# Kernel optimization log

Hardware: AMD Instinct MI355X
Metric: run time of the kernel (lower is better)

## Reference

```python
import jax, jax.numpy as jnp
import numpy as np

B = 4
MAX_N = 2048
D = 512
H = 8
HD = D // H
SRC_LENS = [2048, 1536, 1800, 1200]   # sum = 6584
REF_LENS = [1900, 2048, 1400, 1600]   # sum = 6948
NEG_INF = -1e9


def setup_inputs() -> dict:
    key = jax.random.key(0)
    ks = jax.random.split(key, 8)
    n_src, n_ref = sum(SRC_LENS), sum(REF_LENS)
    s = 0.02
    return {
        "feats_src": jax.random.normal(ks[0], (n_src, D), dtype=jnp.float32),
        "batch_src": jnp.asarray(np.repeat(np.arange(B), SRC_LENS), dtype=jnp.int32),
        "feats_ref": jax.random.normal(ks[1], (n_ref, D), dtype=jnp.float32),
        "batch_ref": jnp.asarray(np.repeat(np.arange(B), REF_LENS), dtype=jnp.int32),
        "w_in": jax.random.normal(ks[2], (3 * D, D), dtype=jnp.float32) * s,
        "b_in": jnp.zeros((3 * D,), dtype=jnp.float32),
        "w_out": jax.random.normal(ks[3], (D, D), dtype=jnp.float32) * s,
        "b_out": jnp.zeros((D,), dtype=jnp.float32),
        "gw1": jax.random.normal(ks[4], (D, D), dtype=jnp.float32) * s,
        "gb1": jnp.zeros((D,), dtype=jnp.float32),
        "gw2": jax.random.normal(ks[5], (1, D), dtype=jnp.float32) * s,
        "gb2": jnp.zeros((1,), dtype=jnp.float32),
    }


def _to_dense(feats, batch_idx):
    # sparse [N, D] (sorted batch indices) -> dense [B, MAX_N, D] + key_padding_mask
    n = feats.shape[0]
    counts = jax.ops.segment_sum(jnp.ones((n,), jnp.int32), batch_idx, num_segments=B)
    starts = jnp.concatenate([jnp.zeros((1,), jnp.int32), jnp.cumsum(counts)[:-1].astype(jnp.int32)])
    pos = jnp.arange(n, dtype=jnp.int32) - starts[batch_idx]  # position within batch
    dense = jnp.zeros((B, MAX_N, feats.shape[1]), feats.dtype).at[batch_idx, pos].set(feats)
    mask = jnp.arange(MAX_N)[None, :] >= counts[:, None]  # True = padding (key_padding_mask)
    return dense, mask, pos


def reference(feats_src, batch_src, feats_ref, batch_ref,
              w_in, b_in, w_out, b_out, gw1, gb1, gw2, gb2):
    d_src, mask_src, pos_src = _to_dense(feats_src, batch_src)
    d_ref, mask_ref, _ = _to_dense(feats_ref, batch_ref)

    # nn.MultiheadAttention (batch_first, eval mode): packed in_proj, scaled dot-product
    q = (d_src @ w_in[:D].T + b_in[:D]).reshape(B, MAX_N, H, HD)
    k = (d_ref @ w_in[D:2 * D].T + b_in[D:2 * D]).reshape(B, MAX_N, H, HD)
    v = (d_ref @ w_in[2 * D:].T + b_in[2 * D:]).reshape(B, MAX_N, H, HD)
    scores = jnp.einsum('bqhd,bkhd->bhqk', q * (HD ** -0.5), k)
    scores = jnp.where(mask_ref[:, None, None, :], NEG_INF, scores)
    attn = jax.nn.softmax(scores, axis=-1)
    ctx = jnp.einsum('bhqk,bkhd->bqhd', attn, v).reshape(B, MAX_N, D)
    d_aligned = ctx @ w_out.T + b_out

    # gate MLP: Linear -> ReLU -> Linear -> Sigmoid
    gate = jax.nn.sigmoid(jax.nn.relu(d_aligned @ gw1.T + gb1) @ gw2.T + gb2)  # [B, MAX_N, 1]
    d_out = d_src + gate * d_aligned

    # dense -> ragged: gather each token back to its flat slot
    out_flat = d_out[batch_src, pos_src]  # [N_src, D]
    return out_flat, gate
```

## Files before the change

kernel.cpp:

```cpp
#include <hip/hip_runtime.h>
#include <hip/hip_bf16.h>


typedef __bf16 bf16x8_t __attribute__((ext_vector_type(8)));
typedef __bf16 bf16x4_t __attribute__((ext_vector_type(4)));
typedef float f32x4_t __attribute__((ext_vector_type(4)));
typedef float f32x2_t __attribute__((ext_vector_type(2)));

#define CQ_SCALE 0.18033688011112042f

__device__ inline bf16x8_t zero8() {
  bf16x8_t z;
#pragma unroll
  for (int t = 0; t < 8; ++t) z[t] = (__bf16)0.0f;
  return z;
}

__device__ __forceinline__ int sniff_f32(const void* w) {
  unsigned short u = ((const unsigned short*)w)[threadIdx.x & 63];
  return __ballot((u & 0x7F80) >= 0x3F80) != 0ULL;
}

__global__ void sentinel_k(float* out) {
  if (threadIdx.x == 0 && blockIdx.x == 0) out[0] = 1000.0f;
}

__global__ void cv_all(const void* w_in, const void* b_in, const void* w_out,
                       const void* b_out, const void* gw1, const void* gb1,
                       const void* gw2, const void* gb2,
                       __hip_bfloat16* __restrict__ ws) {
  int f = sniff_f32(w_in);
  const size_t F_W_IN = 16, F_B_IN = 786448, F_W_OUT = 787984, F_B_OUT = 1050128,
               F_GW1 = 1050640, F_GB1 = 1312784, F_GW2 = 1313296, F_GB2 = 1313808;
  const int total = 1313793;
  for (int g = blockIdx.x * 256 + threadIdx.x; g < total; g += gridDim.x * 256) {
    const void* src;
    size_t dst;
    int i;
    if (g < 786432) { src = w_in; dst = F_W_IN; i = g; }
    else if (g < 787968) { src = b_in; dst = F_B_IN; i = g - 786432; }
    else if (g < 1050112) { src = w_out; dst = F_W_OUT; i = g - 787968; }
    else if (g < 1050624) { src = b_out; dst = F_B_OUT; i = g - 1050112; }
    else if (g < 1312768) { src = gw1; dst = F_GW1; i = g - 1050624; }
    else if (g < 1313280) { src = gb1; dst = F_GB1; i = g - 1312768; }
    else if (g < 1313792) { src = gw2; dst = F_GW2; i = g - 1313280; }
    else { src = gb2; dst = F_GB2; i = g - 1313792; }
    ws[dst + i] = f ? __float2bfloat16(((const float*)src)[i])
                    : ((const __hip_bfloat16*)src)[i];
  }
}

__device__ __forceinline__ void gemm_core(
    const void* __restrict__ A_, long aoff, const __hip_bfloat16* __restrict__ Bt,
    const __hip_bfloat16* __restrict__ bias, __hip_bfloat16* __restrict__ C,
    int M, int K, int lda, int ldc, float cscale, int relu, int f, int bm, int bn,
    long chs, __bf16 (&As)[128][72], __bf16 (&Bs)[128][72]) {
  int tid = threadIdx.x, lane = tid & 63, wave = tid >> 6;
  int wm = wave >> 1, wn = wave & 1;
  int l15 = lane & 15, quad = lane >> 4;

  f32x4_t acc[4][4];
#pragma unroll
  for (int i = 0; i < 4; ++i)
#pragma unroll
    for (int j = 0; j < 4; ++j)
#pragma unroll
      for (int r = 0; r < 4; ++r) acc[i][j][r] = 0.f;

  bf16x8_t ra[4], rb[4];
  f32x4_t raf[4][2];

  auto gload = [&](int k0) {
#pragma unroll
    for (int s = 0; s < 4; ++s) {
      int id = s * 256 + tid;
      int row = id >> 3, col = (id & 7) * 8;
      int arow = bm + row;
      if (f) {
        if (arow < M) {
          const float* p = (const float*)A_ + aoff + (size_t)arow * lda + k0 + col;
          raf[s][0] = *reinterpret_cast<const f32x4_t*>(p);
          raf[s][1] = *reinterpret_cast<const f32x4_t*>(p + 4);
        } else {
#pragma unroll
          for (int e = 0; e < 4; ++e) { raf[s][0][e] = 0.f; raf[s][1][e] = 0.f; }
        }
      } else {
        ra[s] = (arow < M)
                    ? *reinterpret_cast<const bf16x8_t*>((const __hip_bfloat16*)A_ + aoff +
                                                         (size_t)arow * lda + k0 + col)
                    : zero8();
      }
      rb[s] = *reinterpret_cast<const bf16x8_t*>(Bt + (size_t)(bn + row) * 512 + k0 + col);
    }
  };
  auto stage = [&]() {
#pragma unroll
    for (int s = 0; s < 4; ++s) {
      int id = s * 256 + tid;
      int row = id >> 3, col = (id & 7) * 8;
      if (f) {
        bf16x8_t t;
#pragma unroll
        for (int e = 0; e < 4; ++e) {
          t[e] = (__bf16)raf[s][0][e];
          t[4 + e] = (__bf16)raf[s][1][e];
        }
        *reinterpret_cast<bf16x8_t*>(&As[row][col]) = t;
      } else {
        *reinterpret_cast<bf16x8_t*>(&As[row][col]) = ra[s];
      }
      *reinterpret_cast<bf16x8_t*>(&Bs[row][col]) = rb[s];
    }
  };

  int nk = K >> 6;
  gload(0);
  for (int it = 0; it < nk; ++it) {
    stage();
    __syncthreads();
    if (it + 1 < nk) gload((it + 1) * 64);
#pragma unroll
    for (int ks = 0; ks < 2; ++ks) {
      bf16x8_t af[4], bfv[4];
#pragma unroll
      for (int i = 0; i < 4; ++i)
        af[i] = *reinterpret_cast<const bf16x8_t*>(
            &As[wm * 64 + i * 16 + l15][ks * 32 + quad * 8]);
#pragma unroll
      for (int j = 0; j < 4; ++j)
        bfv[j] = *reinterpret_cast<const bf16x8_t*>(
            &Bs[wn * 64 + j * 16 + l15][ks * 32 + quad * 8]);
#pragma unroll
      for (int i = 0; i < 4; ++i)
#pragma unroll
        for (int j = 0; j < 4; ++j)
          acc[i][j] = __builtin_amdgcn_mfma_f32_16x16x32_bf16(af[i], bfv[j], acc[i][j], 0, 0, 0);
    }
    __syncthreads();
  }

#pragma unroll
  for (int i = 0; i < 4; ++i)
#pragma unroll
    for (int j = 0; j < 4; ++j) {
      int col = bn + wn * 64 + j * 16 + l15;
      float bv = __bfloat162float(bias[col]);
#pragma unroll
      for (int r = 0; r < 4; ++r) {
        int row = bm + wm * 64 + i * 16 + quad * 4 + r;
        if (row < M) {
          float v = (acc[i][j][r] + bv) * cscale;
          if (relu) v = fmaxf(v, 0.f);
          size_t idx = chs ? ((size_t)(col >> 6) * chs + (size_t)row * 64 + (col & 63))
                           : ((size_t)row * ldc + col);
          C[idx] = __float2bfloat16(v);
        }
      }
    }
}

__global__ __launch_bounds__(256) void proj2(
    const void* __restrict__ fs, const void* __restrict__ fr,
    const __hip_bfloat16* __restrict__ ws, __hip_bfloat16* __restrict__ Q,
    __hip_bfloat16* __restrict__ KV, const void* snf) {
  __shared__ __bf16 As[128][72];
  __shared__ __bf16 Bs[128][72];
  const size_t F_W_IN = 16, F_B_IN = 786448;
  const long CHS = (long)6948 * 64;
  int f = sniff_f32(snf);
  int bid = blockIdx.x;
  if (bid < 208) {
    int bx = bid >> 2, by = bid & 3;
    gemm_core(fs, 0, ws + F_W_IN, ws + F_B_IN, Q, 6584, 512, 512, 512, CQ_SCALE, 0, f,
              bx * 128, by * 128, 0, As, Bs);
  } else {
    int k = bid - 208;
    int bx = k >> 3, by = k & 7;
    gemm_core(fr, 0, ws + F_W_IN + 262144, ws + F_B_IN + 512, KV, 6948, 512, 512, 1024,
              1.0f, 0, f, bx * 128, by * 128, CHS, As, Bs);
  }
}

template <bool AF32>
__global__ __launch_bounds__(256) void gemm128(
    const void* __restrict__ A_, long aoff, const __hip_bfloat16* __restrict__ Bt,
    const __hip_bfloat16* __restrict__ bias, __hip_bfloat16* __restrict__ C,
    int M, int K, int lda, int ldc, float cscale, int relu, long chs,
    const void* snf) {
  __shared__ __bf16 As[128][72];
  __shared__ __bf16 Bs[128][72];
  int f = 0;
  if constexpr (AF32) f = sniff_f32(snf);
  gemm_core(A_, aoff, Bt, bias, C, M, K, lda, ldc, cscale, relu, f,
            blockIdx.x * 128, blockIdx.y * 128, chs, As, Bs);
}

template <int NS>
__global__ __launch_bounds__(256) void gemm128_pv(
    const __hip_bfloat16* __restrict__ P, const float* __restrict__ L,
    const __hip_bfloat16* __restrict__ Bt, const __hip_bfloat16* __restrict__ bias,
    __hip_bfloat16* __restrict__ C, int M) {
  const size_t PSZ = 3375104;
  __shared__ __bf16 As[128][72];
  __shared__ __bf16 Bs[128][72];
  int tid = threadIdx.x, lane = tid & 63, wave = tid >> 6;
  int wm = wave >> 1, wn = wave & 1;
  int l15 = lane & 15, quad = lane >> 4;
  int bm = blockIdx.x * 128, bn = blockIdx.y * 128;

  f32x4_t acc[4][4];
#pragma unroll
  for (int i = 0; i < 4; ++i)
#pragma unroll
    for (int j = 0; j < 4; ++j)
#pragma unroll
      for (int r = 0; r < 4; ++r) acc[i][j][r] = 0.f;

  bf16x8_t rp[NS][4], rb[4];
  float rl[4][NS];

  auto gload = [&](int k0) {
    int h = k0 >> 6;
#pragma unroll
    for (int s = 0; s < 4; ++s) {
      int id = s * 256 + tid;
      int row = id >> 3, col = (id & 7) * 8;
      int arow = bm + row;
      if (arow < M) {
        size_t off = (size_t)arow * 512 + k0 + col;
#pragma unroll
        for (int i = 0; i < NS; ++i)
          rp[i][s] = *reinterpret_cast<const bf16x8_t*>(P + i * PSZ + off);
        const float* lp = &L[((size_t)arow * 8 + h) * NS];
#pragma unroll
        for (int i = 0; i < NS; ++i) rl[s][i] = lp[i];
      } else {
#pragma unroll
        for (int i = 0; i < NS; ++i) rp[i][s] = zero8();
        rl[s][0] = 1.f;
#pragma unroll
        for (int i = 1; i < NS; ++i) rl[s][i] = 0.f;
      }
      rb[s] = *reinterpret_cast<const bf16x8_t*>(Bt + (size_t)(bn + row) * 512 + k0 + col);
    }
  };
  auto stage = [&]() {
#pragma unroll
    for (int s = 0; s < 4; ++s) {
      int id = s * 256 + tid;
      int row = id >> 3, col = (id & 7) * 8;
      float sum = 0.f;
#pragma unroll
      for (int i = 0; i < NS; ++i) sum += rl[s][i];
      float sc = 1.0f / sum;
      bf16x8_t t;
#pragma unroll
      for (int e = 0; e < 8; ++e) {
        float v = 0.f;
#pragma unroll
        for (int i = 0; i < NS; ++i) v += rl[s][i] * (float)rp[i][s][e];
        t[e] = (__bf16)(v * sc);
      }
      *reinterpret_cast<bf16x8_t*>(&As[row][col]) = t;
      *reinterpret_cast<bf16x8_t*>(&Bs[row][col]) = rb[s];
    }
  };

  gload(0);
  for (int it = 0; it < 8; ++it) {
    stage();
    __syncthreads();
    if (it + 1 < 8) gload((it + 1) * 64);
#pragma unroll
    for (int ks = 0; ks < 2; ++ks) {
      bf16x8_t af[4], bfv[4];
#pragma unroll
      for (int i = 0; i < 4; ++i)
        af[i] = *reinterpret_cast<const bf16x8_t*>(
            &As[wm * 64 + i * 16 + l15][ks * 32 + quad * 8]);
#pragma unroll
      for (int j = 0; j < 4; ++j)
        bfv[j] = *reinterpret_cast<const bf16x8_t*>(
            &Bs[wn * 64 + j * 16 + l15][ks * 32 + quad * 8]);
#pragma unroll
      for (int i = 0; i < 4; ++i)
#pragma unroll
        for (int j = 0; j < 4; ++j)
          acc[i][j] = __builtin_amdgcn_mfma_f32_16x16x32_bf16(af[i], bfv[j], acc[i][j], 0, 0, 0);
    }
    __syncthreads();
  }

#pragma unroll
  for (int i = 0; i < 4; ++i)
#pragma unroll
    for (int j = 0; j < 4; ++j) {
      int col = bn + wn * 64 + j * 16 + l15;
      float bv = __bfloat162float(bias[col]);
#pragma unroll
      for (int r = 0; r < 4; ++r) {
        int row = bm + wm * 64 + i * 16 + quad * 4 + r;
        if (row < M)
          C[(size_t)row * 512 + col] = __float2bfloat16(acc[i][j][r] + bv);
      }
    }
}

__device__ __forceinline__ void flash_core(
    const __hip_bfloat16* __restrict__ Qb, const __hip_bfloat16* __restrict__ Kb,
    const __hip_bfloat16* __restrict__ Vb, __hip_bfloat16* __restrict__ OUTb,
    float* __restrict__ LPb, int lns, int nsrc, int nref, int qt, int kt0,
    int ktNfull, int do_tail, __bf16 (&KsL)[2][64][68], __bf16 (&VtL)[2][64][72],
    __bf16 (&PL)[4][32][68]) {
  int h = blockIdx.y;
  int tid = threadIdx.x, lane = tid & 63, wave = tid >> 6;
  int l15 = lane & 15, quad = lane >> 4;
  int Mb = nsrc + 1;
  int qbase = qt * 128 + wave * 32;

  bf16x8_t qfr[2][2];
#pragma unroll
  for (int g = 0; g < 2; ++g) {
    int qrow = qbase + g * 16 + l15;
#pragma unroll
    for (int ks = 0; ks < 2; ++ks)
      qfr[g][ks] = (qrow < nsrc)
                       ? *reinterpret_cast<const bf16x8_t*>(
                             Qb + (size_t)qrow * 512 + h * 64 + ks * 32 + quad * 8)
                       : zero8();
  }

  f32x4_t O[2][4];
#pragma unroll
  for (int g = 0; g < 2; ++g)
#pragma unroll
    for (int j = 0; j < 4; ++j)
#pragma unroll
      for (int r = 0; r < 4; ++r) O[g][j][r] = 0.f;

  f32x4_t Lacc[2];
#pragma unroll
  for (int g = 0; g < 2; ++g)
#pragma unroll
    for (int r = 0; r < 4; ++r) Lacc[g][r] = 0.f;
  bf16x8_t ones;
#pragma unroll
  for (int t = 0; t < 8; ++t) ones[t] = (__bf16)1.0f;

  auto load64pair = [&](const __bf16* p) {
    bf16x4_t lo = *reinterpret_cast<const bf16x4_t*>(p);
    bf16x4_t hi = *reinterpret_cast<const bf16x4_t*>(p + 4);
    bf16x8_t v;
#pragma unroll
    for (int e = 0; e < 4; ++e) {
      v[e] = lo[e];
      v[4 + e] = hi[e];
    }
    return v;
  };

  bf16x8_t krA[2], v0, v1;
  auto gloadK = [&](int k0) {
    const __hip_bfloat16* base = Kb + (size_t)k0 * 64 + tid * 16;
    krA[0] = *reinterpret_cast<const bf16x8_t*>(base);
    krA[1] = *reinterpret_cast<const bf16x8_t*>(base + 8);
  };
  auto stageK = [&](int buf) {
#pragma unroll
    for (int p = 0; p < 2; ++p) {
      int lin = tid * 16 + p * 8;
      int row = lin >> 6, col = lin & 63;
      *reinterpret_cast<bf16x4_t*>(&KsL[buf][row][col]) =
          *reinterpret_cast<const bf16x4_t*>(&krA[p]);
      bf16x4_t hi;
#pragma unroll
      for (int e = 0; e < 4; ++e) hi[e] = krA[p][4 + e];
      *reinterpret_cast<bf16x4_t*>(&KsL[buf][row][col + 4]) = hi;
    }
  };
  auto loadV = [&](int k0) {
    const __hip_bfloat16* vp = Vb + (size_t)(k0 + lane) * 64 + wave * 16;
    v0 = *reinterpret_cast<const bf16x8_t*>(vp);
    v1 = *reinterpret_cast<const bf16x8_t*>(vp + 8);
  };

  int nit = ktNfull - kt0;
  if (nit > 0) {
    gloadK(kt0 * 64);
    loadV(kt0 * 64);
  }

  int buf = 0;
  for (int it = 0; it < nit; ++it) {
    int k0 = (kt0 + it) * 64;
    stageK(buf);
    {
      __bf16(*Vt)[72] = VtL[buf];
#pragma unroll
      for (int e = 0; e < 8; ++e) {
        Vt[wave * 16 + e][lane] = v0[e];
        Vt[wave * 16 + 8 + e][lane] = v1[e];
      }
    }
    __syncthreads();
    if (it + 1 < nit) {
      gloadK(k0 + 64);
      loadV(k0 + 64);
    }

    bf16x8_t kf[8];
#pragma unroll
    for (int j = 0; j < 4; ++j)
#pragma unroll
      for (int ks = 0; ks < 2; ++ks)
        kf[j * 2 + ks] = load64pair(&KsL[buf][j * 16 + l15][ks * 32 + quad * 8]);
#pragma unroll
    for (int g = 0; g < 2; ++g) {
      f32x4_t St[4];
#pragma unroll
      for (int j = 0; j < 4; ++j)
#pragma unroll
        for (int r = 0; r < 4; ++r) St[j][r] = 0.f;
#pragma unroll
      for (int j = 0; j < 4; ++j)
#pragma unroll
        for (int ks = 0; ks < 2; ++ks)
          St[j] = __builtin_amdgcn_mfma_f32_16x16x32_bf16(kf[j * 2 + ks], qfr[g][ks],
                                                          St[j], 0, 0, 0);
#pragma unroll
      for (int j = 0; j < 4; ++j) {
        bf16x4_t pk;
#pragma unroll
        for (int r = 0; r < 4; ++r) pk[r] = (__bf16)exp2f(St[j][r]);
        *reinterpret_cast<bf16x4_t*>(&PL[wave][g * 16 + l15][j * 16 + quad * 4]) = pk;
      }
    }

    bf16x8_t pa[2][2];
#pragma unroll
    for (int g = 0; g < 2; ++g)
#pragma unroll
      for (int ks = 0; ks < 2; ++ks)
        pa[g][ks] = load64pair(&PL[wave][g * 16 + l15][ks * 32 + quad * 8]);
#pragma unroll
    for (int g = 0; g < 2; ++g)
#pragma unroll
      for (int ks = 0; ks < 2; ++ks)
        Lacc[g] = __builtin_amdgcn_mfma_f32_16x16x32_bf16(pa[g][ks], ones, Lacc[g], 0, 0, 0);
#pragma unroll
    for (int j = 0; j < 4; ++j)
#pragma unroll
      for (int ks = 0; ks < 2; ++ks) {
        bf16x8_t vbf = *reinterpret_cast<const bf16x8_t*>(
            &VtL[buf][j * 16 + l15][ks * 32 + quad * 8]);
#pragma unroll
        for (int g = 0; g < 2; ++g)
          O[g][j] = __builtin_amdgcn_mfma_f32_16x16x32_bf16(pa[g][ks], vbf, O[g][j], 0, 0, 0);
      }
    __syncthreads();
    buf ^= 1;
  }

  if (do_tail) {
    int k0 = ktNfull * 64;
    __bf16(*Vt)[72] = VtL[buf];
    {
      int kr = k0 + lane;
      const __hip_bfloat16* vp = Vb + (size_t)kr * 64 + wave * 16;
      bf16x8_t t0 = (kr < nref) ? *reinterpret_cast<const bf16x8_t*>(vp) : zero8();
      bf16x8_t t1 = (kr < nref) ? *reinterpret_cast<const bf16x8_t*>(vp + 8) : zero8();
#pragma unroll
      for (int e = 0; e < 8; ++e) {
        Vt[wave * 16 + e][lane] = t0[e];
        Vt[wave * 16 + 8 + e][lane] = t1[e];
      }
    }
    bf16x8_t kf[8];
#pragma unroll
    for (int j = 0; j < 4; ++j) {
      int kcol = k0 + j * 16 + l15;
      const __hip_bfloat16* kp = Kb + (size_t)kcol * 64 + quad * 8;
      kf[j * 2] = (kcol < nref) ? *reinterpret_cast<const bf16x8_t*>(kp) : zero8();
      kf[j * 2 + 1] = (kcol < nref) ? *reinterpret_cast<const bf16x8_t*>(kp + 32) : zero8();
    }
#pragma unroll
    for (int g = 0; g < 2; ++g) {
      f32x4_t St[4];
#pragma unroll
      for (int j = 0; j < 4; ++j)
#pragma unroll
        for (int r = 0; r < 4; ++r) St[j][r] = 0.f;
#pragma unroll
      for (int j = 0; j < 4; ++j)
#pragma unroll
        for (int ks = 0; ks < 2; ++ks)
          St[j] = __builtin_amdgcn_mfma_f32_16x16x32_bf16(kf[j * 2 + ks], qfr[g][ks],
                                                          St[j], 0, 0, 0);
#pragma unroll
      for (int j = 0; j < 4; ++j) {
        bf16x4_t pk;
#pragma unroll
        for (int r = 0; r < 4; ++r) {
          int kl = k0 + j * 16 + quad * 4 + r;
          pk[r] = (__bf16)((kl < nref) ? exp2f(St[j][r]) : 0.f);
        }
        *reinterpret_cast<bf16x4_t*>(&PL[wave][g * 16 + l15][j * 16 + quad * 4]) = pk;
      }
    }
    __syncthreads();
    bf16x8_t pa[2][2];
#pragma unroll
    for (int g = 0; g < 2; ++g)
#pragma unroll
      for (int ks = 0; ks < 2; ++ks)
        pa[g][ks] = load64pair(&PL[wave][g * 16 + l15][ks * 32 + quad * 8]);
#pragma unroll
    for (int g = 0; g < 2; ++g)
#pragma unroll
      for (int ks = 0; ks < 2; ++ks)
        Lacc[g] = __builtin_amdgcn_mfma_f32_16x16x32_bf16(pa[g][ks], ones, Lacc[g], 0, 0, 0);
#pragma unroll
    for (int j = 0; j < 4; ++j)
#pragma unroll
      for (int ks = 0; ks < 2; ++ks) {
        bf16x8_t vbf =
            *reinterpret_cast<const bf16x8_t*>(&Vt[j * 16 + l15][ks * 32 + quad * 8]);
#pragma unroll
        for (int g = 0; g < 2; ++g)
          O[g][j] = __builtin_amdgcn_mfma_f32_16x16x32_bf16(pa[g][ks], vbf, O[g][j], 0, 0, 0);
      }
  }

  if (LPb && l15 == 0) {
#pragma unroll
    for (int g = 0; g < 2; ++g)
#pragma unroll
      for (int r = 0; r < 4; ++r) {
        int row = qbase + g * 16 + quad * 4 + r;
        if (row < Mb) LPb[((size_t)row * 8 + h) * lns] = Lacc[g][r];
      }
  }

#pragma unroll
  for (int g = 0; g < 2; ++g)
#pragma unroll
    for (int r = 0; r < 4; ++r) {
      int row = qbase + g * 16 + quad * 4 + r;
      if (row < Mb) {
        float inv = 1.0f / Lacc[g][r];
#pragma unroll
        for (int j = 0; j < 4; ++j)
          OUTb[(size_t)row * 512 + h * 64 + j * 16 + l15] =
              __float2bfloat16(O[g][j][r] * inv);
      }
    }
}

__global__ __launch_bounds__(256, 3) void flash_all(
    const __hip_bfloat16* __restrict__ Q, const __hip_bfloat16* __restrict__ KV,
    __hip_bfloat16* __restrict__ P, float* __restrict__ L, int nsplit) {
  const int TILE_START[4] = {0, 17, 30, 45};
  const int SRC_START[4] = {0, 2048, 3584, 5384};
  const int REF_START[4] = {0, 1900, 3948, 5348};
  const int SRC_LEN[4] = {2048, 1536, 1800, 1200};
  const int REF_LEN[4] = {1900, 2048, 1400, 1600};
  const int CS[4] = {0, 2049, 3586, 5387};
  const size_t PSZ = 3375104;
  const size_t CHS = (size_t)6948 * 64;
  __shared__ __bf16 KsL[2][64][68];
  __shared__ __bf16 VtL[2][64][72];
  __shared__ __bf16 PL[4][32][68];
  int bid = blockIdx.x;
  int b = (bid >= TILE_START[3]) ? 3 : (bid >= TILE_START[2]) ? 2 : (bid >= TILE_START[1]) ? 1 : 0;
  int qt = bid - TILE_START[b];
  int nref = REF_LEN[b];
  int full = nref >> 6, nkt = (nref + 63) >> 6, rem = nref & 63;
  int split = blockIdx.z;
  int kt0 = (nkt * split) / nsplit;
  int ktN, tail;
  if (split == nsplit - 1) { ktN = full; tail = rem > 0; }
  else { ktN = (nkt * (split + 1)) / nsplit; tail = 0; }
  int h = blockIdx.y;
  const __hip_bfloat16* Kb = KV + (size_t)h * CHS + (size_t)REF_START[b] * 64;
  const __hip_bfloat16* Vb = KV + (size_t)(8 + h) * CHS + (size_t)REF_START[b] * 64;
  __hip_bfloat16* OUT = P + (size_t)split * PSZ;
  float* LP = (nsplit == 1) ? nullptr : (L + split + (size_t)CS[b] * 8 * nsplit);
  flash_core(Q + (size_t)SRC_START[b] * 512, Kb, Vb, OUT + (size_t)CS[b] * 512, LP,
             nsplit, SRC_LEN[b], nref, qt, kt0, ktN, tail, KsL, VtL, PL);
}

__global__ __launch_bounds__(256, 3) void flash_one(const __hip_bfloat16* __restrict__ Qb,
                                                    const __hip_bfloat16* __restrict__ KVb,
                                                    __hip_bfloat16* __restrict__ OUTb,
                                                    int nsrc, int nref, long chs) {
  __shared__ __bf16 KsL[2][64][68];
  __shared__ __bf16 VtL[2][64][72];
  __shared__ __bf16 PL[4][32][68];
  int h = blockIdx.y;
  const __hip_bfloat16* Kb = KVb + (size_t)h * chs;
  const __hip_bfloat16* Vb = KVb + (size_t)(8 + h) * chs;
  flash_core(Qb, Kb, Vb, OUTb, nullptr, 1, nsrc, nref, blockIdx.x, 0, nref >> 6,
             (nref & 63) > 0, KsL, VtL, PL);
}

__global__ __launch_bounds__(256) void finalize_all(
    const void* __restrict__ src, const __hip_bfloat16* __restrict__ aligned,
    const __hip_bfloat16* __restrict__ hidden, const __hip_bfloat16* __restrict__ gw2,
    const __hip_bfloat16* __restrict__ gb2, void* __restrict__ out, const void* snf) {
  int f = sniff_f32(snf);
  int lane = threadIdx.x & 63;
  int r = blockIdx.x * 4 + (threadIdx.x >> 6);
  int b = (r >= 5387) ? 3 : (r >= 3586) ? 2 : (r >= 2049) ? 1 : 0;
  const int CS[4] = {0, 2049, 3586, 5387};
  const int NSRC[4] = {2048, 1536, 1800, 1200};
  int pos = r - CS[b];

  float zacc = 0.f;
  const __hip_bfloat16* hrow = hidden + (size_t)r * 512;
#pragma unroll
  for (int t = 0; t < 8; ++t) {
    int c = lane + (t << 6);
    zacc += __bfloat162float(hrow[c]) * __bfloat162float(gw2[c]);
  }
  for (int o = 32; o; o >>= 1) zacc += __shfl_xor(zacc, o);
  zacc += __bfloat162float(gb2[0]);
  float g = 1.f / (1.f + __expf(-zacc));

  const size_t GOFF = (size_t)6584 * 512;
  if (pos < NSRC[b]) {
    size_t ib = (size_t)(r - b) * 512;
    const __hip_bfloat16* arow = aligned + (size_t)r * 512;
#pragma unroll
    for (int t = 0; t < 8; ++t) {
      int c = lane + (t << 6);
      float sv = f ? ((const float*)src)[ib + c]
                   : __bfloat162float(((const __hip_bfloat16*)src)[ib + c]);
      float val = sv + g * __bfloat162float(arow[c]);
      if (f) ((float*)out)[ib + c] = val;
      else ((__hip_bfloat16*)out)[ib + c] = __float2bfloat16(val);
    }
    if (lane == 0) {
      size_t go = GOFF + b * 2048 + pos;
      if (f) ((float*)out)[go] = g;
      else ((__hip_bfloat16*)out)[go] = __float2bfloat16(g);
    }
  } else {
    for (int p = NSRC[b] + lane; p < 2048; p += 64) {
      size_t go = GOFF + b * 2048 + p;
      if (f) ((float*)out)[go] = g;
      else ((__hip_bfloat16*)out)[go] = __float2bfloat16(g);
    }
  }
}

__global__ __launch_bounds__(256) void finalize_b(
    const void* __restrict__ src, const __hip_bfloat16* __restrict__ alnb,
    const __hip_bfloat16* __restrict__ hidb, const __hip_bfloat16* __restrict__ gw2,
    const __hip_bfloat16* __restrict__ gb2, void* __restrict__ out,
    int b, int nsrc, int src_start, const void* snf) {
  int f = sniff_f32(snf);
  int lane = threadIdx.x & 63;
  int r = blockIdx.x * 4 + (threadIdx.x >> 6);
  if (r > nsrc) return;

  float zacc = 0.f;
  const __hip_bfloat16* hrow = hidb + (size_t)r * 512;
#pragma unroll
  for (int t = 0; t < 8; ++t) {
    int c = lane + (t << 6);
    zacc += __bfloat162float(hrow[c]) * __bfloat162float(gw2[c]);
  }
  for (int o = 32; o; o >>= 1) zacc += __shfl_xor(zacc, o);
  zacc += __bfloat162float(gb2[0]);
  float g = 1.f / (1.f + __expf(-zacc));

  const size_t GOFF = (size_t)6584 * 512;
  if (r < nsrc) {
    size_t ib = (size_t)(src_start + r) * 512;
    const __hip_bfloat16* arow = alnb + (size_t)r * 512;
#pragma unroll
    for (int t = 0; t < 8; ++t) {
      int c = lane + (t << 6);
      float sv = f ? ((const float*)src)[ib + c]
                   : __bfloat162float(((const __hip_bfloat16*)src)[ib + c]);
      float val = sv + g * __bfloat162float(arow[c]);
      if (f) ((float*)out)[ib + c] = val;
      else ((__hip_bfloat16*)out)[ib + c] = __float2bfloat16(val);
    }
    if (lane == 0) {
      size_t go = GOFF + b * 2048 + r;
      if (f) ((float*)out)[go] = g;
      else ((__hip_bfloat16*)out)[go] = __float2bfloat16(g);
    }
  } else {
    for (int p = nsrc + lane; p < 2048; p += 64) {
      size_t go = GOFF + b * 2048 + p;
      if (f) ((float*)out)[go] = g;
      else ((__hip_bfloat16*)out)[go] = __float2bfloat16(g);
    }
  }
}

extern "C" void kernel_launch(void* const* d_in, const int* in_sizes, int n_in,
                              void* d_out, int out_size, void* d_ws, size_t ws_size,
                              hipStream_t stream) {
  (void)in_sizes; (void)n_in; (void)out_size;
  const void* feats_src = d_in[0];
  const void* feats_ref = d_in[2];
  const void* w_in = d_in[4];
  const void* b_in = d_in[5];
  const void* w_out = d_in[6];
  const void* b_out = d_in[7];
  const void* gw1 = d_in[8];
  const void* gb1 = d_in[9];
  const void* gw2 = d_in[10];
  const void* gb2 = d_in[11];

  const size_t F_W_IN = 16, F_B_IN = 786448, F_W_OUT = 787984, F_B_OUT = 1050128,
               F_GW1 = 1050640, F_GB1 = 1312784, F_GW2 = 1313296, F_GB2 = 1313808,
               A0 = 1313824;
  const size_t PSZ = 3375104;
  const size_t R3E = A0 + PSZ + 7114752;
  const size_t NEED_A2 = 2 * (R3E + 2 * PSZ + 210816);
  const size_t NEED_A = 2 * (R3E + PSZ);
  const size_t NEED_B = 2 * (A0 + 4259840);

  if (ws_size < NEED_B) {
    sentinel_k<<<1, 64, 0, stream>>>((float*)d_out);
    return;
  }

  __hip_bfloat16* ws = (__hip_bfloat16*)d_ws;
  cv_all<<<dim3(1024), dim3(256), 0, stream>>>(w_in, b_in, w_out, b_out, gw1, gb1, gw2,
                                               gb2, ws);

  const int SRC_LEN[4] = {2048, 1536, 1800, 1200};
  const int REF_LEN[4] = {1900, 2048, 1400, 1600};
  const int SRC_START[4] = {0, 2048, 3584, 5384};
  const int REF_START[4] = {0, 1900, 3948, 5348};
  dim3 blk(256);

  if (ws_size >= NEED_A) {
    __hip_bfloat16* R1 = ws + A0;
    __hip_bfloat16* R2 = R1 + PSZ;
    __hip_bfloat16* R3 = R2 + 7114752;
    proj2<<<dim3(648), blk, 0, stream>>>(feats_src, feats_ref, ws, R1, R2, w_in);
    int NS = (ws_size >= NEED_A2) ? 2 : 1;
    if (NS == 2) {
      float* L = (float*)(ws + R3E + 2 * PSZ);
      flash_all<<<dim3(55, 8, 2), blk, 0, stream>>>(R1, R2, R3, L, 2);
      gemm128_pv<2><<<dim3(52, 4), blk, 0, stream>>>(R3, L, ws + F_W_OUT,
                                                     ws + F_B_OUT, R1, 6588);
    } else {
      flash_all<<<dim3(55, 8, 1), blk, 0, stream>>>(R1, R2, R3, nullptr, 1);
      gemm128<false><<<dim3(52, 4), blk, 0, stream>>>(R3, 0, ws + F_W_OUT, ws + F_B_OUT,
                                                      R1, 6588, 512, 512, 512, 1.0f, 0,
                                                      0, nullptr);
    }
    gemm128<false><<<dim3(52, 4), blk, 0, stream>>>(R1, 0, ws + F_GW1, ws + F_GB1, R3,
                                                    6588, 512, 512, 512, 1.0f, 1, 0,
                                                    nullptr);
    finalize_all<<<dim3(1647), blk, 0, stream>>>(feats_src, R1, R3, ws + F_GW2,
                                                 ws + F_GB2, d_out, w_in);
  } else {
    __hip_bfloat16* W2 = ws + A0;
    __hip_bfloat16* W1 = W2 + 2097152;
    __hip_bfloat16* W3 = W1 + 1081344;
    const long CHS_B = (long)2048 * 64;
    for (int b = 0; b < 4; ++b) {
      int nsrc = SRC_LEN[b], nref = REF_LEN[b];
      gemm128<true><<<dim3((nsrc + 127) / 128, 4), blk, 0, stream>>>(
          feats_src, (long)SRC_START[b] * 512, ws + F_W_IN, ws + F_B_IN, W1, nsrc, 512,
          512, 512, CQ_SCALE, 0, 0, w_in);
      gemm128<true><<<dim3((nref + 127) / 128, 8), blk, 0, stream>>>(
          feats_ref, (long)REF_START[b] * 512, ws + F_W_IN + 262144, ws + F_B_IN + 512,
          W2, nref, 512, 512, 1024, 1.0f, 0, CHS_B, w_in);
      flash_one<<<dim3((nsrc + 128) / 128, 8), blk, 0, stream>>>(W1, W2, W3, nsrc, nref,
                                                                 CHS_B);
      gemm128<false><<<dim3((nsrc + 128) / 128, 4), blk, 0, stream>>>(
          W3, 0, ws + F_W_OUT, ws + F_B_OUT, W1, nsrc + 1, 512, 512, 512, 1.0f, 0, 0,
          nullptr);
      gemm128<false><<<dim3((nsrc + 128) / 128, 4), blk, 0, stream>>>(
          W1, 0, ws + F_GW1, ws + F_GB1, W3, nsrc + 1, 512, 512, 512, 1.0f, 1, 0,
          nullptr);
      finalize_b<<<dim3((nsrc + 4) / 4), blk, 0, stream>>>(
          feats_src, W1, W3, ws + F_GW2, ws + F_GB2, d_out, b, nsrc, SRC_START[b], w_in);
    }
  }
}
```

Baseline: 236.6 us.

## Shrink GEMM N-tile to 64 and split flash launch by batch pairs

Changes every GEMM tile from 128x128 to 128x64, with each of the four waves owning 32 rows. Grids double and the kernels get launch_bounds min-blocks of 4, so more blocks fit on the GPU and occupancy rises on these small-M GEMMs. The flash attention launch is split into two launches, one per pair of batches, with the tile-to-batch lookup rewritten to match. The cost is less B-operand reuse per block, more redundant A loads, and one extra kernel launch.

```diff
diff --git a/kernel.cpp b/kernel.cpp
--- a/kernel.cpp
+++ b/kernel.cpp
@@ -54,20 +54,19 @@
     const void* __restrict__ A_, long aoff, const __hip_bfloat16* __restrict__ Bt,
     const __hip_bfloat16* __restrict__ bias, __hip_bfloat16* __restrict__ C,
     int M, int K, int lda, int ldc, float cscale, int relu, int f, int bm, int bn,
-    long chs, __bf16 (&As)[128][72], __bf16 (&Bs)[128][72]) {
+    long chs, __bf16 (&As)[128][72], __bf16 (&Bs)[64][72]) {
   int tid = threadIdx.x, lane = tid & 63, wave = tid >> 6;
-  int wm = wave >> 1, wn = wave & 1;
   int l15 = lane & 15, quad = lane >> 4;
 
-  f32x4_t acc[4][4];
-#pragma unroll
-  for (int i = 0; i < 4; ++i)
+  f32x4_t acc[2][4];
+#pragma unroll
+  for (int i = 0; i < 2; ++i)
 #pragma unroll
     for (int j = 0; j < 4; ++j)
 #pragma unroll
       for (int r = 0; r < 4; ++r) acc[i][j][r] = 0.f;
 
-  bf16x8_t ra[4], rb[4];
+  bf16x8_t ra[4], rb[2];
   f32x4_t raf[4][2];
 
   auto gload = [&](int k0) {
@@ -91,6 +90,11 @@
                                                          (size_t)arow * lda + k0 + col)
                     : zero8();
       }
+    }
+#pragma unroll
+    for (int s = 0; s < 2; ++s) {
+      int id = s * 256 + tid;
+      int row = id >> 3, col = (id & 7) * 8;
       rb[s] = *reinterpret_cast<const bf16x8_t*>(Bt + (size_t)(bn + row) * 512 + k0 + col);
     }
   };
@@ -110,6 +114,11 @@
       } else {
         *reinterpret_cast<bf16x8_t*>(&As[row][col]) = ra[s];
       }
+    }
+#pragma unroll
+    for (int s = 0; s < 2; ++s) {
+      int id = s * 256 + tid;
+      int row = id >> 3, col = (id & 7) * 8;
       *reinterpret_cast<bf16x8_t*>(&Bs[row][col]) = rb[s];
     }
   };
@@ -122,17 +131,17 @@
     if (it + 1 < nk) gload((it + 1) * 64);
 #pragma unroll
     for (int ks = 0; ks < 2; ++ks) {
-      bf16x8_t af[4], bfv[4];
-#pragma unroll
-      for (int i = 0; i < 4; ++i)
+      bf16x8_t af[2], bfv[4];
+#pragma unroll
+      for (int i = 0; i < 2; ++i)
         af[i] = *reinterpret_cast<const bf16x8_t*>(
-            &As[wm * 64 + i * 16 + l15][ks * 32 + quad * 8]);
+            &As[wave * 32 + i * 16 + l15][ks * 32 + quad * 8]);
 #pragma unroll
       for (int j = 0; j < 4; ++j)
         bfv[j] = *reinterpret_cast<const bf16x8_t*>(
-            &Bs[wn * 64 + j * 16 + l15][ks * 32 + quad * 8]);
-#pragma unroll
-      for (int i = 0; i < 4; ++i)
+            &Bs[j * 16 + l15][ks * 32 + quad * 8]);
+#pragma unroll
+      for (int i = 0; i < 2; ++i)
 #pragma unroll
         for (int j = 0; j < 4; ++j)
           acc[i][j] = __builtin_amdgcn_mfma_f32_16x16x32_bf16(af[i], bfv[j], acc[i][j], 0, 0, 0);
@@ -141,14 +150,14 @@
   }
 
 #pragma unroll
-  for (int i = 0; i < 4; ++i)
+  for (int i = 0; i < 2; ++i)
 #pragma unroll
     for (int j = 0; j < 4; ++j) {
-      int col = bn + wn * 64 + j * 16 + l15;
+      int col = bn + j * 16 + l15;
       float bv = __bfloat162float(bias[col]);
 #pragma unroll
       for (int r = 0; r < 4; ++r) {
-        int row = bm + wm * 64 + i * 16 + quad * 4 + r;
+        int row = bm + wave * 32 + i * 16 + quad * 4 + r;
         if (row < M) {
           float v = (acc[i][j][r] + bv) * cscale;
           if (relu) v = fmaxf(v, 0.f);
@@ -160,64 +169,63 @@
     }
 }
 
-__global__ __launch_bounds__(256) void proj2(
+__global__ __launch_bounds__(256, 4) void proj2(
     const void* __restrict__ fs, const void* __restrict__ fr,
     const __hip_bfloat16* __restrict__ ws, __hip_bfloat16* __restrict__ Q,
     __hip_bfloat16* __restrict__ KV, const void* snf) {
   __shared__ __bf16 As[128][72];
-  __shared__ __bf16 Bs[128][72];
+  __shared__ __bf16 Bs[64][72];
   const size_t F_W_IN = 16, F_B_IN = 786448;
   const long CHS = (long)6948 * 64;
   int f = sniff_f32(snf);
   int bid = blockIdx.x;
-  if (bid < 208) {
-    int bx = bid >> 2, by = bid & 3;
+  if (bid < 416) {
+    int bx = bid >> 3, by = bid & 7;
     gemm_core(fs, 0, ws + F_W_IN, ws + F_B_IN, Q, 6584, 512, 512, 512, CQ_SCALE, 0, f,
-              bx * 128, by * 128, 0, As, Bs);
+              bx * 128, by * 64, 0, As, Bs);
   } else {
-    int k = bid - 208;
-    int bx = k >> 3, by = k & 7;
+    int k = bid - 416;
+    int bx = k >> 4, by = k & 15;
     gemm_core(fr, 0, ws + F_W_IN + 262144, ws + F_B_IN + 512, KV, 6948, 512, 512, 1024,
-              1.0f, 0, f, bx * 128, by * 128, CHS, As, Bs);
+              1.0f, 0, f, bx * 128, by * 64, CHS, As, Bs);
   }
 }
 
 template <bool AF32>
-__global__ __launch_bounds__(256) void gemm128(
+__global__ __launch_bounds__(256, 4) void gemm128(
     const void* __restrict__ A_, long aoff, const __hip_bfloat16* __restrict__ Bt,
     const __hip_bfloat16* __restrict__ bias, __hip_bfloat16* __restrict__ C,
     int M, int K, int lda, int ldc, float cscale, int relu, long chs,
     const void* snf) {
   __shared__ __bf16 As[128][72];
-  __shared__ __bf16 Bs[128][72];
+  __shared__ __bf16 Bs[64][72];
   int f = 0;
   if constexpr (AF32) f = sniff_f32(snf);
   gemm_core(A_, aoff, Bt, bias, C, M, K, lda, ldc, cscale, relu, f,
-            blockIdx.x * 128, blockIdx.y * 128, chs, As, Bs);
+            blockIdx.x * 128, blockIdx.y * 64, chs, As, Bs);
 }
 
 template <int NS>
-__global__ __launch_bounds__(256) void gemm128_pv(
+__global__ __launch_bounds__(256, 4) void gemm128_pv(
     const __hip_bfloat16* __restrict__ P, const float* __restrict__ L,
     const __hip_bfloat16* __restrict__ Bt, const __hip_bfloat16* __restrict__ bias,
     __hip_bfloat16* __restrict__ C, int M) {
   const size_t PSZ = 3375104;
   __shared__ __bf16 As[128][72];
-  __shared__ __bf16 Bs[128][72];
+  __shared__ __bf16 Bs[64][72];
   int tid = threadIdx.x, lane = tid & 63, wave = tid >> 6;
-  int wm = wave >> 1, wn = wave & 1;
   int l15 = lane & 15, quad = lane >> 4;
-  int bm = blockIdx.x * 128, bn = blockIdx.y * 128;
-
-  f32x4_t acc[4][4];
-#pragma unroll
-  for (int i = 0; i < 4; ++i)
+  int bm = blockIdx.x * 128, bn = blockIdx.y * 64;
+
+  f32x4_t acc[2][4];
+#pragma unroll
+  for (int i = 0; i < 2; ++i)
 #pragma unroll
     for (int j = 0; j < 4; ++j)
 #pragma unroll
       for (int r = 0; r < 4; ++r) acc[i][j][r] = 0.f;
 
-  bf16x8_t rp[NS][4], rb[4];
+  bf16x8_t rp[NS][4], rb[2];
   float rl[4][NS];
 
   auto gload = [&](int k0) {
@@ -242,6 +250,11 @@
 #pragma unroll
         for (int i = 1; i < NS; ++i) rl[s][i] = 0.f;
       }
+    }
+#pragma unroll
+    for (int s = 0; s < 2; ++s) {
+      int id = s * 256 + tid;
+      int row = id >> 3, col = (id & 7) * 8;
       rb[s] = *reinterpret_cast<const bf16x8_t*>(Bt + (size_t)(bn + row) * 512 + k0 + col);
     }
   };
@@ -263,6 +276,11 @@
         t[e] = (__bf16)(v * sc);
       }
       *reinterpret_cast<bf16x8_t*>(&As[row][col]) = t;
+    }
+#pragma unroll
+    for (int s = 0; s < 2; ++s) {
+      int id = s * 256 + tid;
+      int row = id >> 3, col = (id & 7) * 8;
       *reinterpret_cast<bf16x8_t*>(&Bs[row][col]) = rb[s];
     }
   };
@@ -274,17 +292,17 @@
     if (it + 1 < 8) gload((it + 1) * 64);
 #pragma unroll
     for (int ks = 0; ks < 2; ++ks) {
-      bf16x8_t af[4], bfv[4];
-#pragma unroll
-      for (int i = 0; i < 4; ++i)
+      bf16x8_t af[2], bfv[4];
+#pragma unroll
+      for (int i = 0; i < 2; ++i)
         af[i] = *reinterpret_cast<const bf16x8_t*>(
-            &As[wm * 64 + i * 16 + l15][ks * 32 + quad * 8]);
+            &As[wave * 32 + i * 16 + l15][ks * 32 + quad * 8]);
 #pragma unroll
       for (int j = 0; j < 4; ++j)
         bfv[j] = *reinterpret_cast<const bf16x8_t*>(
-            &Bs[wn * 64 + j * 16 + l15][ks * 32 + quad * 8]);
-#pragma unroll
-      for (int i = 0; i < 4; ++i)
+            &Bs[j * 16 + l15][ks * 32 + quad * 8]);
+#pragma unroll
+      for (int i = 0; i < 2; ++i)
 #pragma unroll
         for (int j = 0; j < 4; ++j)
           acc[i][j] = __builtin_amdgcn_mfma_f32_16x16x32_bf16(af[i], bfv[j], acc[i][j], 0, 0, 0);
@@ -293,14 +311,14 @@
   }
 
 #pragma unroll
-  for (int i = 0; i < 4; ++i)
+  for (int i = 0; i < 2; ++i)
 #pragma unroll
     for (int j = 0; j < 4; ++j) {
-      int col = bn + wn * 64 + j * 16 + l15;
+      int col = bn + j * 16 + l15;
       float bv = __bfloat162float(bias[col]);
 #pragma unroll
       for (int r = 0; r < 4; ++r) {
-        int row = bm + wm * 64 + i * 16 + quad * 4 + r;
+        int row = bm + wave * 32 + i * 16 + quad * 4 + r;
         if (row < M)
           C[(size_t)row * 512 + col] = __float2bfloat16(acc[i][j][r] + bv);
       }
@@ -559,8 +577,8 @@
 
 __global__ __launch_bounds__(256, 3) void flash_all(
     const __hip_bfloat16* __restrict__ Q, const __hip_bfloat16* __restrict__ KV,
-    __hip_bfloat16* __restrict__ P, float* __restrict__ L, int nsplit) {
-  const int TILE_START[4] = {0, 17, 30, 45};
+    __hip_bfloat16* __restrict__ P, float* __restrict__ L, int bpair, int nsplit) {
+  const int SPLIT_T[2] = {17, 15};
   const int SRC_START[4] = {0, 2048, 3584, 5384};
   const int REF_START[4] = {0, 1900, 3948, 5348};
   const int SRC_LEN[4] = {2048, 1536, 1800, 1200};
@@ -571,9 +589,10 @@
   __shared__ __bf16 KsL[2][64][68];
   __shared__ __bf16 VtL[2][64][72];
   __shared__ __bf16 PL[4][32][68];
-  int bid = blockIdx.x;
-  int b = (bid >= TILE_START[3]) ? 3 : (bid >= TILE_START[2]) ? 2 : (bid >= TILE_START[1]) ? 1 : 0;
-  int qt = bid - TILE_START[b];
+  int local = blockIdx.x;
+  int half = (local >= SPLIT_T[bpair]) ? 1 : 0;
+  int b = bpair * 2 + half;
+  int qt = local - (half ? SPLIT_T[bpair] : 0);
   int nref = REF_LEN[b];
   int full = nref >> 6, nkt = (nref + 63) >> 6, rem = nref & 63;
   int split = blockIdx.z;
@@ -745,20 +764,22 @@
     __hip_bfloat16* R1 = ws + A0;
     __hip_bfloat16* R2 = R1 + PSZ;
     __hip_bfloat16* R3 = R2 + 7114752;
-    proj2<<<dim3(648), blk, 0, stream>>>(feats_src, feats_ref, ws, R1, R2, w_in);
+    proj2<<<dim3(1296), blk, 0, stream>>>(feats_src, feats_ref, ws, R1, R2, w_in);
     int NS = (ws_size >= NEED_A2) ? 2 : 1;
     if (NS == 2) {
       float* L = (float*)(ws + R3E + 2 * PSZ);
-      flash_all<<<dim3(55, 8, 2), blk, 0, stream>>>(R1, R2, R3, L, 2);
-      gemm128_pv<2><<<dim3(52, 4), blk, 0, stream>>>(R3, L, ws + F_W_OUT,
+      flash_all<<<dim3(30, 8, 2), blk, 0, stream>>>(R1, R2, R3, L, 0, 2);
+      flash_all<<<dim3(25, 8, 2), blk, 0, stream>>>(R1, R2, R3, L, 1, 2);
+      gemm128_pv<2><<<dim3(52, 8), blk, 0, stream>>>(R3, L, ws + F_W_OUT,
                                                      ws + F_B_OUT, R1, 6588);
     } else {
-      flash_all<<<dim3(55, 8, 1), blk, 0, stream>>>(R1, R2, R3, nullptr, 1);
-      gemm128<false><<<dim3(52, 4), blk, 0, stream>>>(R3, 0, ws + F_W_OUT, ws + F_B_OUT,
+      flash_all<<<dim3(30, 8, 1), blk, 0, stream>>>(R1, R2, R3, nullptr, 0, 1);
+      flash_all<<<dim3(25, 8, 1), blk, 0, stream>>>(R1, R2, R3, nullptr, 1, 1);
+      gemm128<false><<<dim3(52, 8), blk, 0, stream>>>(R3, 0, ws + F_W_OUT, ws + F_B_OUT,
                                                       R1, 6588, 512, 512, 512, 1.0f, 0,
                                                       0, nullptr);
     }
-    gemm128<false><<<dim3(52, 4), blk, 0, stream>>>(R1, 0, ws + F_GW1, ws + F_GB1, R3,
+    gemm128<false><<<dim3(52, 8), blk, 0, stream>>>(R1, 0, ws + F_GW1, ws + F_GB1, R3,
                                                     6588, 512, 512, 512, 1.0f, 1, 0,
                                                     nullptr);
     finalize_all<<<dim3(1647), blk, 0, stream>>>(feats_src, R1, R3, ws + F_GW2,
@@ -770,18 +791,18 @@
     const long CHS_B = (long)2048 * 64;
     for (int b = 0; b < 4; ++b) {
       int nsrc = SRC_LEN[b], nref = REF_LEN[b];
-      gemm128<true><<<dim3((nsrc + 127) / 128, 4), blk, 0, stream>>>(
+      gemm128<true><<<dim3((nsrc + 127) / 128, 8), blk, 0, stream>>>(
           feats_src, (long)SRC_START[b] * 512, ws + F_W_IN, ws + F_B_IN, W1, nsrc, 512,
           512, 512, CQ_SCALE, 0, 0, w_in);
-      gemm128<true><<<dim3((nref + 127) / 128, 8), blk, 0, stream>>>(
+      gemm128<true><<<dim3((nref + 127) / 128, 16), blk, 0, stream>>>(
           feats_ref, (long)REF_START[b] * 512, ws + F_W_IN + 262144, ws + F_B_IN + 512,
           W2, nref, 512, 512, 1024, 1.0f, 0, CHS_B, w_in);
       flash_one<<<dim3((nsrc + 128) / 128, 8), blk, 0, stream>>>(W1, W2, W3, nsrc, nref,
                                                                  CHS_B);
-      gemm128<false><<<dim3((nsrc + 128) / 128, 4), blk, 0, stream>>>(
+      gemm128<false><<<dim3((nsrc + 128) / 128, 8), blk, 0, stream>>>(
           W3, 0, ws + F_W_OUT, ws + F_B_OUT, W1, nsrc + 1, 512, 512, 512, 1.0f, 0, 0,
           nullptr);
-      gemm128<false><<<dim3((nsrc + 128) / 128, 4), blk, 0, stream>>>(
+      gemm128<false><<<dim3((nsrc + 128) / 128, 8), blk, 0, stream>>>(
           W1, 0, ws + F_GW1, ws + F_GB1, W3, nsrc + 1, 512, 512, 512, 1.0f, 1, 0,
           nullptr);
       finalize_b<<<dim3((nsrc + 4) / 4), blk, 0, stream>>>(
```

Measured after the change: 260.5 us. 10.1% more time.

## Pre-convert features to bf16 and swizzle GEMM block mapping for L2 locality

Applied to the files above, without the earlier changes.

Adds a cv_feats kernel that converts src/ref features to bf16 in workspace before the projection GEMM, so proj2 reads bf16 A operands instead of converting fp32 on load. All 128x128 GEMMs use a 1D grid with an XCD-aware swizzle (bid&7 spread) so blocks sharing A/B tiles land on the same XCD's L2. The pre-conversion adds an extra kernel launch and a memory pass over the features in exchange for cheaper GEMM loads.

```diff
diff --git a/kernel.cpp b/kernel.cpp
--- a/kernel.cpp
+++ b/kernel.cpp
@@ -19,6 +19,12 @@
 __device__ __forceinline__ int sniff_f32(const void* w) {
   unsigned short u = ((const unsigned short*)w)[threadIdx.x & 63];
   return __ballot((u & 0x7F80) >= 0x3F80) != 0ULL;
+}
+
+__device__ __forceinline__ int2 swz(int bid, int nwg, int nby) {
+  int chunk = nwg >> 3;
+  int w = (bid & 7) * chunk + (bid >> 3);
+  return make_int2(w / nby, w % nby);
 }
 
 __global__ void sentinel_k(float* out) {
@@ -50,6 +56,30 @@
   }
 }
 
+__global__ __launch_bounds__(256) void cv_feats(const void* fs, const void* fr,
+                                                __hip_bfloat16* __restrict__ ws,
+                                                const void* snf) {
+  int f = sniff_f32(snf);
+  int i = blockIdx.x * 256 + threadIdx.x;
+  const int NFS = 421376;
+  const void* src;
+  size_t dst;
+  int off;
+  if (i < NFS) { src = fs; dst = 11803680; off = i * 8; }
+  else { src = fr; dst = 15174688; off = (i - NFS) * 8; }
+  __hip_bfloat16* d = ws + dst + off;
+  if (f) {
+    const float* p = (const float*)src + off;
+    bf16x8_t v;
+#pragma unroll
+    for (int e = 0; e < 8; ++e) v[e] = (__bf16)p[e];
+    *reinterpret_cast<bf16x8_t*>(d) = v;
+  } else {
+    *reinterpret_cast<bf16x8_t*>(d) =
+        *reinterpret_cast<const bf16x8_t*>((const __hip_bfloat16*)src + off);
+  }
+}
+
 __device__ __forceinline__ void gemm_core(
     const void* __restrict__ A_, long aoff, const __hip_bfloat16* __restrict__ Bt,
     const __hip_bfloat16* __restrict__ bias, __hip_bfloat16* __restrict__ C,
@@ -168,18 +198,28 @@
   __shared__ __bf16 Bs[128][72];
   const size_t F_W_IN = 16, F_B_IN = 786448;
   const long CHS = (long)6948 * 64;
-  int f = sniff_f32(snf);
+  int f = snf ? sniff_f32(snf) : 0;
   int bid = blockIdx.x;
   if (bid < 208) {
-    int bx = bid >> 2, by = bid & 3;
+    int2 s = swz(bid, 208, 4);
     gemm_core(fs, 0, ws + F_W_IN, ws + F_B_IN, Q, 6584, 512, 512, 512, CQ_SCALE, 0, f,
-              bx * 128, by * 128, 0, As, Bs);
+              s.x * 128, s.y * 128, 0, As, Bs);
   } else {
-    int k = bid - 208;
-    int bx = k >> 3, by = k & 7;
+    int2 s = swz(bid - 208, 440, 8);
     gemm_core(fr, 0, ws + F_W_IN + 262144, ws + F_B_IN + 512, KV, 6948, 512, 512, 1024,
-              1.0f, 0, f, bx * 128, by * 128, CHS, As, Bs);
-  }
+              1.0f, 0, f, s.x * 128, s.y * 128, CHS, As, Bs);
+  }
+}
+
+__global__ __launch_bounds__(256) void gemm128z(
+    const __hip_bfloat16* __restrict__ A, const __hip_bfloat16* __restrict__ Bt,
+    const __hip_bfloat16* __restrict__ bias, __hip_bfloat16* __restrict__ C,
+    int M, float cscale, int relu) {
+  __shared__ __bf16 As[128][72];
+  __shared__ __bf16 Bs[128][72];
+  int2 s = swz(blockIdx.x, gridDim.x, 4);
+  gemm_core(A, 0, Bt, bias, C, M, 512, 512, 512, cscale, relu, 0,
+            s.x * 128, s.y * 128, 0, As, Bs);
 }
 
 template <bool AF32>
@@ -207,7 +247,8 @@
   int tid = threadIdx.x, lane = tid & 63, wave = tid >> 6;
   int wm = wave >> 1, wn = wave & 1;
   int l15 = lane & 15, quad = lane >> 4;
-  int bm = blockIdx.x * 128, bn = blockIdx.y * 128;
+  int2 sw = swz(blockIdx.x, 208, 4);
+  int bm = sw.x * 128, bn = sw.y * 128;
 
   f32x4_t acc[4][4];
 #pragma unroll
@@ -722,6 +763,8 @@
                A0 = 1313824;
   const size_t PSZ = 3375104;
   const size_t R3E = A0 + PSZ + 7114752;
+  const size_t FS0 = R3E;
+  const size_t FR0 = R3E + 3371008;
   const size_t NEED_A2 = 2 * (R3E + 2 * PSZ + 210816);
   const size_t NEED_A = 2 * (R3E + PSZ);
   const size_t NEED_B = 2 * (A0 + 4259840);
@@ -745,22 +788,22 @@
     __hip_bfloat16* R1 = ws + A0;
     __hip_bfloat16* R2 = R1 + PSZ;
     __hip_bfloat16* R3 = R2 + 7114752;
-    proj2<<<dim3(648), blk, 0, stream>>>(feats_src, feats_ref, ws, R1, R2, w_in);
     int NS = (ws_size >= NEED_A2) ? 2 : 1;
     if (NS == 2) {
+      cv_feats<<<dim3(3383), blk, 0, stream>>>(feats_src, feats_ref, ws, w_in);
+      proj2<<<dim3(648), blk, 0, stream>>>(ws + FS0, ws + FR0, ws, R1, R2, nullptr);
       float* L = (float*)(ws + R3E + 2 * PSZ);
       flash_all<<<dim3(55, 8, 2), blk, 0, stream>>>(R1, R2, R3, L, 2);
-      gemm128_pv<2><<<dim3(52, 4), blk, 0, stream>>>(R3, L, ws + F_W_OUT,
-                                                     ws + F_B_OUT, R1, 6588);
+      gemm128_pv<2><<<dim3(208), blk, 0, stream>>>(R3, L, ws + F_W_OUT,
+                                                   ws + F_B_OUT, R1, 6588);
     } else {
+      proj2<<<dim3(648), blk, 0, stream>>>(feats_src, feats_ref, ws, R1, R2, w_in);
       flash_all<<<dim3(55, 8, 1), blk, 0, stream>>>(R1, R2, R3, nullptr, 1);
-      gemm128<false><<<dim3(52, 4), blk, 0, stream>>>(R3, 0, ws + F_W_OUT, ws + F_B_OUT,
-                                                      R1, 6588, 512, 512, 512, 1.0f, 0,
-                                                      0, nullptr);
-    }
-    gemm128<false><<<dim3(52, 4), blk, 0, stream>>>(R1, 0, ws + F_GW1, ws + F_GB1, R3,
-                                                    6588, 512, 512, 512, 1.0f, 1, 0,
-                                                    nullptr);
+      gemm128z<<<dim3(208), blk, 0, stream>>>(R3, ws + F_W_OUT, ws + F_B_OUT, R1,
+                                              6588, 1.0f, 0);
+    }
+    gemm128z<<<dim3(208), blk, 0, stream>>>(R1, ws + F_GW1, ws + F_GB1, R3, 6588,
+                                            1.0f, 1);
     finalize_all<<<dim3(1647), blk, 0, stream>>>(feats_src, R1, R3, ws + F_GW2,
                                                  ws + F_GB2, d_out, w_in);
   } else {
```

New measurement: 238.5 us. No clear change (+0.8%).
